# Kernel tuning notes

Measured on AMD Instinct MI355X. Metric: run time of the kernel, lower is better.

## Reference

```python
import jax, jax.numpy as jnp
from jax import lax
import numpy as np

H = 8          # n_heads
K = 4          # n_points == KNN k (hardcoded k=4 in original)
NN = 4         # neighbors per sampling point
D_MODEL = 256


def setup_inputs() -> dict:
    key = jax.random.key(0)
    ks = jax.random.split(key, 16)
    b, n_q, n_kv, d = 2, 1024, 2048, D_MODEL
    query = jax.random.normal(ks[0], (b, n_q, d), dtype=jnp.float32)
    query_pos = jax.random.uniform(ks[1], (b, n_q, 2), dtype=jnp.float32)
    key_value = jax.random.normal(ks[2], (b, n_kv, d), dtype=jnp.float32)
    kv_pos = jax.random.uniform(ks[3], (b, n_kv, 2), dtype=jnp.float32)
    # sampling_offsets linear: small weights + rotated-grid bias (as in _reset_parameters, scaled
    # so sampling locations stay near the unit square of kv positions)
    W_off = 0.001 * jax.random.normal(ks[4], (d, H * K * 2), dtype=jnp.float32)
    thetas = np.arange(H, dtype=np.float32) * (2.0 * np.pi / H)
    grid = np.stack([np.cos(thetas), np.sin(thetas)], -1)          # [H,2]
    grid = grid / np.abs(grid).max(-1, keepdims=True)
    grid = np.repeat(grid[:, None, :], K, axis=1)                  # [H,K,2]
    grid = grid * (np.arange(1, K + 1, dtype=np.float32)[None, :, None])
    b_off = jnp.asarray(0.05 * grid.reshape(-1), dtype=jnp.float32)
    W_attn = 0.02 * jax.random.normal(ks[5], (d, H * K), dtype=jnp.float32)
    b_attn = jnp.zeros((H * K,), dtype=jnp.float32)
    xav = (6.0 / (d + d)) ** 0.5
    W_v = jax.random.uniform(ks[6], (d, d), minval=-xav, maxval=xav, dtype=jnp.float32)
    b_v = jnp.zeros((d,), dtype=jnp.float32)
    W_out = jax.random.uniform(ks[7], (d, d), minval=-xav, maxval=xav, dtype=jnp.float32)
    b_out = jnp.zeros((d,), dtype=jnp.float32)
    shepard_power = jnp.asarray(1.0, dtype=jnp.float32)
    return {"query": query, "query_pos": query_pos, "key_value": key_value, "kv_pos": kv_pos,
            "W_off": W_off, "b_off": b_off, "W_attn": W_attn, "b_attn": b_attn,
            "W_v": W_v, "b_v": b_v, "W_out": W_out, "b_out": b_out,
            "shepard_power": shepard_power}


def _deform_attn(query, query_pos, key_value, kv_pos,
                 W_off, b_off, W_attn, b_attn, W_v, b_v, W_out, b_out, shepard_power):
    b, n_q, c = query.shape
    n_kv = key_value.shape[1]
    c_ = c // H
    # projections
    off = (query @ W_off + b_off).reshape(b, n_q, H, K, 2)
    attn = jax.nn.softmax((query @ W_attn + b_attn).reshape(b, n_q, H, K), axis=-1)
    values = (key_value @ W_v + b_v).reshape(b, n_kv, H, c_)
    values = values.transpose(0, 2, 1, 3).reshape(b * H, n_kv, c_)
    # sampling locations [b*H, n_q*K, 2]
    loc = (query_pos[:, :, None, None, :] + off).transpose(0, 2, 1, 3, 4)
    loc = loc.reshape(b * H, n_q * K, 2)
    kvp = jnp.broadcast_to(kv_pos[:, None], (b, H, n_kv, 2)).reshape(b * H, n_kv, 2)
    # brute-force KNN (k=4) on squared distances via GEMM expansion
    d2 = ((loc * loc).sum(-1)[:, :, None] + (kvp * kvp).sum(-1)[:, None, :]
          - 2.0 * jnp.einsum('bqd,bkd->bqk', loc, kvp))           # [bH, nqK, n_kv]
    _, nb_idx = lax.top_k(-d2, NN)                                 # [bH, nqK, 4]
    bidx = jnp.arange(b * H)[:, None, None]
    nb_pos = kvp[bidx, nb_idx]                                     # [bH, nqK, 4, 2]
    dist = jnp.linalg.norm(nb_pos - loc[:, :, None, :], axis=-1) + 1e-6
    power = jax.nn.relu(shepard_power) + 1e-6
    nn_w = jax.nn.softmax(-power * dist, axis=-1)                  # Shepard weights over 4 nbrs
    nn_w = nn_w.reshape(b * H, n_q, K, NN)
    idx = nb_idx.reshape(b * H, n_q, K, NN)
    attn_r = attn.transpose(0, 2, 1, 3).reshape(b * H, n_q, K)
    vg = values[jnp.arange(b * H)[:, None, None, None], idx]       # [bH, n_q, K, 4, c_]
    out = jnp.einsum('bqp,bqpn,bqpnc->bqc', attn_r, nn_w, vg)      # [bH, n_q, c_]
    out = out.reshape(b, H, n_q, c_).transpose(0, 2, 1, 3).reshape(b, n_q, c)
    return out @ W_out + b_out


def reference(query, query_pos, key_value, kv_pos,
              W_off, b_off, W_attn, b_attn, W_v, b_v, W_out, b_out, shepard_power):
    return _deform_attn(query, query_pos, key_value, kv_pos,
                        W_off, b_off, W_attn, b_attn, W_v, b_v, W_out, b_out, shepard_power)
```

## Files before the change

kernel.cpp:

```cpp
#include <hip/hip_runtime.h>
#include <math.h>

#define H 8
#define K 4
#define NN 4
#define D 256
#define NQ 1024
#define NKV 2048
#define BATCH 2
#define CH 32
#define GC 16
#define CELLH 0.0625f

#define OFF_LOC   0u
#define OFF_ATTN  524288u
#define OFF_VWS   786432u
#define OFF_HEAD  4980736u
#define OFF_PTS   7077888u
#define OFF_CST   7143424u
#define WS_NEED   7147520u

__global__ void k_offattn(const float* __restrict__ q, const float* __restrict__ qpos,
                          const float* __restrict__ Woff, const float* __restrict__ boff,
                          const float* __restrict__ Wattn, const float* __restrict__ battn,
                          float* __restrict__ loc, float* __restrict__ attnw) {
    int row = blockIdx.x;
    int b = row >> 10, qi = row & (NQ - 1);
    __shared__ float qs[D];
    for (int d = threadIdx.x; d < D; d += blockDim.x) qs[d] = q[(size_t)row * D + d];
    __syncthreads();
    int j = threadIdx.x;
    if (j < 64) {
        float acc = 0.0f;
        for (int d = 0; d < D; ++d) acc = fmaf(qs[d], Woff[d * 64 + j], acc);
        float off = acc + boff[j];
        int xy = j & 1;
        int hk = j >> 1;
        int h = hk >> 2, k = hk & 3;
        float L = qpos[(size_t)row * 2 + xy] + off;
        int g = ((b * H + h) * NQ + qi) * K + k;
        loc[(size_t)g * 2 + xy] = L;
    } else if (j < 96) {
        int j2 = j - 64;
        float acc = 0.0f;
        for (int d = 0; d < D; ++d) acc = fmaf(qs[d], Wattn[d * 32 + j2], acc);
        acc += battn[j2];
        float m = acc;
        m = fmaxf(m, __shfl_xor(m, 1));
        m = fmaxf(m, __shfl_xor(m, 2));
        float e = expf(acc - m);
        float s = e;
        s += __shfl_xor(s, 1);
        s += __shfl_xor(s, 2);
        float w = e / s;
        int h = j2 >> 2, k = j2 & 3;
        attnw[((b * H + h) * NQ + qi) * K + k] = w;
    }
}

__global__ void k_values(const float* __restrict__ kv, const float* __restrict__ Wv,
                         const float* __restrict__ bv, float* __restrict__ vws) {
    int r0 = blockIdx.x * 4;
    __shared__ float ks[4][D];
    for (int t = threadIdx.x; t < 4 * D; t += 256) ks[t >> 8][t & 255] = kv[(size_t)r0 * D + t];
    __syncthreads();
    int c = threadIdx.x;
    float a0 = 0.f, a1 = 0.f, a2 = 0.f, a3 = 0.f;
    for (int d = 0; d < D; ++d) {
        float w = Wv[d * D + c];
        a0 = fmaf(ks[0][d], w, a0); a1 = fmaf(ks[1][d], w, a1);
        a2 = fmaf(ks[2][d], w, a2); a3 = fmaf(ks[3][d], w, a3);
    }
    float bias = bv[c];
    a0 += bias; a1 += bias; a2 += bias; a3 += bias;
    int h = c >> 5, cc = c & 31;
    float va[4] = {a0, a1, a2, a3};
    for (int r = 0; r < 4; ++r) {
        int row = r0 + r;
        int b = row >> 11, n = row & (NKV - 1);
        vws[(((size_t)(b * H + h) * NKV) + n) * CH + cc] = va[r];
    }
}

__global__ void k_bin(const float* __restrict__ kvpos, float4* __restrict__ pts4,
                      int* __restrict__ cellStart) {
    #pragma clang fp contract(off)
    int b = blockIdx.x;
    int tid = threadIdx.x;
    __shared__ int cnt[GC * GC];
    __shared__ int ofs[GC * GC + 1];
    __shared__ int cur[GC * GC];
    if (tid < GC * GC) cnt[tid] = 0;
    __syncthreads();
    for (int n = tid; n < NKV; n += 256) {
        float x = kvpos[(size_t)(b * NKV + n) * 2 + 0];
        float y = kvpos[(size_t)(b * NKV + n) * 2 + 1];
        int ix = min(GC - 1, max(0, (int)floorf(x * (float)GC)));
        int iy = min(GC - 1, max(0, (int)floorf(y * (float)GC)));
        atomicAdd(&cnt[iy * GC + ix], 1);
    }
    __syncthreads();
    if (tid == 0) {
        int s = 0;
        for (int c = 0; c < GC * GC; ++c) { ofs[c] = s; s += cnt[c]; }
        ofs[GC * GC] = s;
    }
    __syncthreads();
    for (int t = tid; t < GC * GC + 1; t += 256) cellStart[b * 257 + t] = ofs[t];
    if (tid < GC * GC) cur[tid] = ofs[tid];
    __syncthreads();
    for (int n = tid; n < NKV; n += 256) {
        float x = kvpos[(size_t)(b * NKV + n) * 2 + 0];
        float y = kvpos[(size_t)(b * NKV + n) * 2 + 1];
        int ix = min(GC - 1, max(0, (int)floorf(x * (float)GC)));
        int iy = min(GC - 1, max(0, (int)floorf(y * (float)GC)));
        int pos = atomicAdd(&cur[iy * GC + ix], 1);
        pts4[(size_t)b * NKV + pos] = make_float4(-2.0f * x, -2.0f * y, x * x + y * y, (float)n);
    }
}

__device__ __forceinline__ void lexins(float t, int n,
                                       float& d0, float& d1, float& d2, float& d3,
                                       int& i0, int& i1, int& i2, int& i3) {
    bool c0 = (t < d0) || (t == d0 && n < i0);
    bool c1 = (t < d1) || (t == d1 && n < i1);
    bool c2 = (t < d2) || (t == d2 && n < i2);
    bool c3 = (t < d3) || (t == d3 && n < i3);
    d3 = c3 ? (c2 ? d2 : t) : d3;   i3 = c3 ? (c2 ? i2 : n) : i3;
    d2 = c2 ? (c1 ? d1 : t) : d2;   i2 = c2 ? (c1 ? i1 : n) : i2;
    d1 = c1 ? (c0 ? d0 : t) : d1;   i1 = c1 ? (c0 ? i0 : n) : i1;
    d0 = c0 ? t : d0;               i0 = c0 ? n : i0;
}

__device__ __forceinline__ void lexins_d(float t, int n,
                                         float& d0, float& d1, float& d2, float& d3,
                                         int& i0, int& i1, int& i2, int& i3) {
    bool nd = !((n == i0) | (n == i1) | (n == i2) | (n == i3));
    bool c0 = nd && ((t < d0) || (t == d0 && n < i0));
    bool c1 = nd && ((t < d1) || (t == d1 && n < i1));
    bool c2 = nd && ((t < d2) || (t == d2 && n < i2));
    bool c3 = nd && ((t < d3) || (t == d3 && n < i3));
    d3 = c3 ? (c2 ? d2 : t) : d3;   i3 = c3 ? (c2 ? i2 : n) : i3;
    d2 = c2 ? (c1 ? d1 : t) : d2;   i2 = c2 ? (c1 ? i1 : n) : i2;
    d1 = c1 ? (c0 ? d0 : t) : d1;   i1 = c1 ? (c0 ? i0 : n) : i1;
    d0 = c0 ? t : d0;               i0 = c0 ? n : i0;
}

__device__ __forceinline__ void bins4(float t, int n,
                                      float& d0, float& d1, float& d2, float& d3,
                                      int& i0, int& i1, int& i2, int& i3) {
    bool c0 = t < d0, c1 = t < d1, c2 = t < d2, c3 = t < d3;
    d3 = c3 ? (c2 ? d2 : t) : d3;   i3 = c3 ? (c2 ? i2 : n) : i3;
    d2 = c2 ? (c1 ? d1 : t) : d2;   i2 = c2 ? (c1 ? i1 : n) : i2;
    d1 = c1 ? (c0 ? d0 : t) : d1;   i1 = c1 ? (c0 ? i0 : n) : i1;
    d0 = c0 ? t : d0;               i0 = c0 ? n : i0;
}

__device__ __forceinline__ void knn_tail(int g, float lx, float ly,
                                         int i0, int i1, int i2, int i3,
                                         const float* __restrict__ kvpos,
                                         const float* __restrict__ attnw,
                                         const float* __restrict__ vws,
                                         float power, float* __restrict__ head) {
    #pragma clang fp contract(off)
    int bh = g >> 12;
    int b = bh >> 3, h = bh & 7;
    int qi = (g >> 2) & (NQ - 1);
    int k = g & 3;
    int idx[4] = {i0, i1, i2, i3};
    float z[4];
    #pragma unroll
    for (int u = 0; u < 4; ++u) {
        float kx = kvpos[(size_t)(b * NKV + idx[u]) * 2 + 0];
        float ky = kvpos[(size_t)(b * NKV + idx[u]) * 2 + 1];
        float dx = kx - lx;
        float dy = ky - ly;
        float dist = sqrtf(dx * dx + dy * dy) + 1e-6f;
        z[u] = -power * dist;
    }
    float m = fmaxf(fmaxf(z[0], z[1]), fmaxf(z[2], z[3]));
    float e0 = expf(z[0] - m), e1 = expf(z[1] - m), e2 = expf(z[2] - m), e3 = expf(z[3] - m);
    float esum = e0 + e1 + e2 + e3;
    float w0 = e0 / esum, w1 = e1 / esum, w2 = e2 / esum, w3 = e3 / esum;

    const float4* vp0 = (const float4*)(vws + ((size_t)bh * NKV + i0) * CH);
    const float4* vp1 = (const float4*)(vws + ((size_t)bh * NKV + i1) * CH);
    const float4* vp2 = (const float4*)(vws + ((size_t)bh * NKV + i2) * CH);
    const float4* vp3 = (const float4*)(vws + ((size_t)bh * NKV + i3) * CH);
    float a = attnw[g];
    float4 acc[8];
    #pragma unroll
    for (int t = 0; t < 8; ++t) {
        float4 x0 = vp0[t], x1 = vp1[t], x2 = vp2[t], x3 = vp3[t];
        float4 r;
        r.x = a * (w0 * x0.x + w1 * x1.x + w2 * x2.x + w3 * x3.x);
        r.y = a * (w0 * x0.y + w1 * x1.y + w2 * x2.y + w3 * x3.y);
        r.z = a * (w0 * x0.z + w1 * x1.z + w2 * x2.z + w3 * x3.z);
        r.w = a * (w0 * x0.w + w1 * x1.w + w2 * x2.w + w3 * x3.w);
        r.x += __shfl_xor(r.x, 1); r.x += __shfl_xor(r.x, 2);
        r.y += __shfl_xor(r.y, 1); r.y += __shfl_xor(r.y, 2);
        r.z += __shfl_xor(r.z, 1); r.z += __shfl_xor(r.z, 2);
        r.w += __shfl_xor(r.w, 1); r.w += __shfl_xor(r.w, 2);
        acc[t] = r;
    }
    float4* hp = (float4*)(head + ((size_t)(b * NQ + qi)) * D + h * CH);
    hp[k * 2]     = acc[k * 2];
    hp[k * 2 + 1] = acc[k * 2 + 1];
}

__global__ void k_knn_grid2(const float* __restrict__ kvpos, const float* __restrict__ loc,
                            const float* __restrict__ attnw, const float* __restrict__ vws,
                            const float* __restrict__ sp,
                            const float4* __restrict__ pts4, const int* __restrict__ cellStart,
                            float* __restrict__ head) {
    #pragma clang fp contract(off)
    int lane = threadIdx.x;
    int s = lane & 7;
    int g = blockIdx.x * 32 + (lane >> 3);
    int b = g >> 15;
    int bh = g >> 12;

    __shared__ int cst[GC * GC + 1];
    for (int i = threadIdx.x; i < GC * GC + 1; i += 256) cst[i] = cellStart[b * 257 + i];
    __syncthreads();

    const float4* gp = pts4 + (size_t)b * NKV;

    const float2* lp = (const float2*)loc;
    float2 L = lp[g];
    float lx = L.x, ly = L.y;
    float sl = lx * lx + ly * ly;

    int ix = min(GC - 1, max(0, (int)floorf(lx * (float)GC)));
    int iy = min(GC - 1, max(0, (int)floorf(ly * (float)GC)));

    float d0 = 1e30f, d1 = 1e30f, d2 = 1e30f, d3 = 1e30f;
    int i0 = 0x7FFFFFFF, i1 = 0x7FFFFFFF, i2 = 0x7FFFFFFF, i3 = 0x7FFFFFFF;

#define INS1(P) { float tt = (sl + (P).z) + fmaf(ly, (P).y, lx * (P).x);      \
                  lexins(tt, (int)(P).w, d0, d1, d2, d3, i0, i1, i2, i3); }

    {
        int bx0 = max(ix - 1, 0), bx1 = min(ix + 1, GC - 1);
        int by0 = max(iy - 1, 0), by1 = min(iy + 1, GC - 1);
        int a0 = cst[by0 * GC + bx0];
        int l0 = cst[by0 * GC + bx1 + 1] - a0;
        int a1 = 0, l1 = 0, a2 = 0, l2 = 0;
        if (by0 + 1 <= by1) { a1 = cst[(by0 + 1) * GC + bx0]; l1 = cst[(by0 + 1) * GC + bx1 + 1] - a1; }
        if (by0 + 2 <= by1) { a2 = cst[(by0 + 2) * GC + bx0]; l2 = cst[(by0 + 2) * GC + bx1 + 1] - a2; }
        int l01 = l0 + l1;
        int m = l01 + l2;
        int f = s;
        for (; f + 24 < m; f += 32) {
            int f0 = f, f1 = f + 8, f2 = f + 16, f3 = f + 24;
            int j0 = f0 < l0 ? a0 + f0 : (f0 < l01 ? a1 + (f0 - l0) : a2 + (f0 - l01));
            int j1 = f1 < l0 ? a0 + f1 : (f1 < l01 ? a1 + (f1 - l0) : a2 + (f1 - l01));
            int j2 = f2 < l0 ? a0 + f2 : (f2 < l01 ? a1 + (f2 - l0) : a2 + (f2 - l01));
            int j3 = f3 < l0 ? a0 + f3 : (f3 < l01 ? a1 + (f3 - l0) : a2 + (f3 - l01));
            float4 p0 = gp[j0], p1 = gp[j1], p2 = gp[j2], p3 = gp[j3];
            INS1(p0); INS1(p1); INS1(p2); INS1(p3);
        }
        for (; f < m; f += 8) {
            int j = f < l0 ? a0 + f : (f < l01 ? a1 + (f - l0) : a2 + (f - l01));
            float4 p = gp[j];
            INS1(p);
        }
    }

#define MERGE_P(M) {                                                           \
        float e0 = __shfl_xor(d0, M), e1 = __shfl_xor(d1, M);                  \
        float e2 = __shfl_xor(d2, M), e3 = __shfl_xor(d3, M);                  \
        int j0 = __shfl_xor(i0, M), j1 = __shfl_xor(i1, M);                    \
        int j2 = __shfl_xor(i2, M), j3 = __shfl_xor(i3, M);                    \
        lexins(e0, j0, d0, d1, d2, d3, i0, i1, i2, i3);                        \
        lexins(e1, j1, d0, d1, d2, d3, i0, i1, i2, i3);                        \
        lexins(e2, j2, d0, d1, d2, d3, i0, i1, i2, i3);                        \
        lexins(e3, j3, d0, d1, d2, d3, i0, i1, i2, i3);                        \
    }
#define MERGE_D(M) {                                                           \
        float e0 = __shfl_xor(d0, M), e1 = __shfl_xor(d1, M);                  \
        float e2 = __shfl_xor(d2, M), e3 = __shfl_xor(d3, M);                  \
        int j0 = __shfl_xor(i0, M), j1 = __shfl_xor(i1, M);                    \
        int j2 = __shfl_xor(i2, M), j3 = __shfl_xor(i3, M);                    \
        lexins_d(e0, j0, d0, d1, d2, d3, i0, i1, i2, i3);                      \
        lexins_d(e1, j1, d0, d1, d2, d3, i0, i1, i2, i3);                      \
        lexins_d(e2, j2, d0, d1, d2, d3, i0, i1, i2, i3);                      \
        lexins_d(e3, j3, d0, d1, d2, d3, i0, i1, i2, i3);                      \
    }

    MERGE_P(1);
    MERGE_P(2);
    MERGE_P(4);

    auto done_at = [&](int r) -> bool {
        int bx0 = ix - r, bx1 = ix + r, by0 = iy - r, by1 = iy + r;
        float bound = 1e30f;
        if (bx0 > 0)      bound = fminf(bound, lx - (float)bx0 * CELLH);
        if (bx1 < GC - 1) bound = fminf(bound, (float)(bx1 + 1) * CELLH - lx);
        if (by0 > 0)      bound = fminf(bound, ly - (float)by0 * CELLH);
        if (by1 < GC - 1) bound = fminf(bound, (float)(by1 + 1) * CELLH - ly);
        bool covered = (bx0 <= 0 && bx1 >= GC - 1 && by0 <= 0 && by1 >= GC - 1);
        return covered || (d3 < bound * bound - 1e-5f);
    };

#define SCAN_RANGE_S(JLO, JHI)                                       \
    for (int j = (JLO) + s; j < (JHI); j += 8) {                     \
        float4 p = gp[j];                                            \
        INS1(p);                                                     \
    }

    int r = 1;
    bool need = !done_at(1);
    while (__any(need)) {
        ++r;
        if (need) {
            int ry0 = iy - r, ry1 = iy + r;
            int rx0 = ix - r, rx1 = ix + r;
            int ca = max(rx0, 0), cb = min(rx1, GC - 1);
            if (ry0 >= 0)      { int base = ry0 * GC; SCAN_RANGE_S(cst[base + ca], cst[base + cb + 1]); }
            if (ry1 <= GC - 1) { int base = ry1 * GC; SCAN_RANGE_S(cst[base + ca], cst[base + cb + 1]); }
            int ya = max(ry0 + 1, 0), yb = min(ry1 - 1, GC - 1);
            if (rx0 >= 0)      for (int cy = ya; cy <= yb; ++cy) { int c = cy * GC + rx0; SCAN_RANGE_S(cst[c], cst[c + 1]); }
            if (rx1 <= GC - 1) for (int cy = ya; cy <= yb; ++cy) { int c = cy * GC + rx1; SCAN_RANGE_S(cst[c], cst[c + 1]); }
            MERGE_D(1);
            MERGE_D(2);
            MERGE_D(4);
            need = !done_at(r);
        }
    }
#undef SCAN_RANGE_S
#undef MERGE_P
#undef MERGE_D
#undef INS1

    int bb = bh >> 3, h = bh & 7;
    int qi = (g >> 2) & (NQ - 1);
    float power = fmaxf(sp[0], 0.0f) + 1e-6f;
    int idx[4] = {i0, i1, i2, i3};
    float z[4];
    #pragma unroll
    for (int u = 0; u < 4; ++u) {
        float kx = kvpos[(size_t)(bb * NKV + idx[u]) * 2 + 0];
        float ky = kvpos[(size_t)(bb * NKV + idx[u]) * 2 + 1];
        float dx = kx - lx;
        float dy = ky - ly;
        float dist = sqrtf(dx * dx + dy * dy) + 1e-6f;
        z[u] = -power * dist;
    }
    float m = fmaxf(fmaxf(z[0], z[1]), fmaxf(z[2], z[3]));
    float e0 = expf(z[0] - m), e1 = expf(z[1] - m), e2 = expf(z[2] - m), e3 = expf(z[3] - m);
    float esum = e0 + e1 + e2 + e3;
    float w0 = e0 / esum, w1 = e1 / esum, w2 = e2 / esum, w3 = e3 / esum;

    const float4* vp0 = (const float4*)(vws + ((size_t)bh * NKV + i0) * CH);
    const float4* vp1 = (const float4*)(vws + ((size_t)bh * NKV + i1) * CH);
    const float4* vp2 = (const float4*)(vws + ((size_t)bh * NKV + i2) * CH);
    const float4* vp3 = (const float4*)(vws + ((size_t)bh * NKV + i3) * CH);
    float a = attnw[g];
    float4* hp = (float4*)(head + ((size_t)(bb * NQ + qi)) * D + h * CH);
    {
        float4 x0 = vp0[s], x1 = vp1[s], x2 = vp2[s], x3 = vp3[s];
        float4 rr;
        rr.x = a * (w0 * x0.x + w1 * x1.x + w2 * x2.x + w3 * x3.x);
        rr.y = a * (w0 * x0.y + w1 * x1.y + w2 * x2.y + w3 * x3.y);
        rr.z = a * (w0 * x0.z + w1 * x1.z + w2 * x2.z + w3 * x3.z);
        rr.w = a * (w0 * x0.w + w1 * x1.w + w2 * x2.w + w3 * x3.w);
        rr.x += __shfl_xor(rr.x, 8); rr.x += __shfl_xor(rr.x, 16);
        rr.y += __shfl_xor(rr.y, 8); rr.y += __shfl_xor(rr.y, 16);
        rr.z += __shfl_xor(rr.z, 8); rr.z += __shfl_xor(rr.z, 16);
        rr.w += __shfl_xor(rr.w, 8); rr.w += __shfl_xor(rr.w, 16);
        if (((lane >> 3) & 3) == 0) hp[s] = rr;
    }
}

__global__ void k_knn_fused(const float* __restrict__ kvpos, const float* __restrict__ loc,
                            const float* __restrict__ attnw, const float* __restrict__ vws,
                            const float* __restrict__ sp, float* __restrict__ head) {
    #pragma clang fp contract(off)
    int g = blockIdx.x * 256 + threadIdx.x;
    int bh = g >> 12;
    int b = bh >> 3;
    __shared__ float sx[NKV];
    __shared__ float sy[NKV];
    __shared__ float sz[NKV];
    for (int n = threadIdx.x; n < NKV; n += 256) {
        float x = kvpos[(size_t)(b * NKV + n) * 2 + 0];
        float y = kvpos[(size_t)(b * NKV + n) * 2 + 1];
        sx[n] = -2.0f * x;
        sy[n] = -2.0f * y;
        sz[n] = x * x + y * y;
    }
    __syncthreads();
    const float2* lp = (const float2*)loc;
    float2 L = lp[g];
    float lx = L.x, ly = L.y;
    float sl = lx * lx + ly * ly;
    const float4* x4 = (const float4*)sx;
    const float4* y4 = (const float4*)sy;
    const float4* z4 = (const float4*)sz;
    float d0 = 1e30f, d1 = 1e30f, d2 = 1e30f, d3 = 1e30f;
    int i0 = 0, i1 = 0, i2 = 0, i3 = 0;
    for (int n = 0; n < NKV; n += 4) {
        int v = n >> 2;
        float4 xA = x4[v], yA = y4[v], zA = z4[v];
        float t0 = (sl + zA.x) + fmaf(ly, yA.x, lx * xA.x);
        float t1 = (sl + zA.y) + fmaf(ly, yA.y, lx * xA.y);
        float t2 = (sl + zA.z) + fmaf(ly, yA.z, lx * xA.z);
        float t3 = (sl + zA.w) + fmaf(ly, yA.w, lx * xA.w);
        bins4(t0, n + 0, d0, d1, d2, d3, i0, i1, i2, i3);
        bins4(t1, n + 1, d0, d1, d2, d3, i0, i1, i2, i3);
        bins4(t2, n + 2, d0, d1, d2, d3, i0, i1, i2, i3);
        bins4(t3, n + 3, d0, d1, d2, d3, i0, i1, i2, i3);
    }
    float power = fmaxf(sp[0], 0.0f) + 1e-6f;
    knn_tail(g, lx, ly, i0, i1, i2, i3, kvpos, attnw, vws, power, head);
}

__global__ void k_out(const float* __restrict__ head, const float* __restrict__ Wout,
                      const float* __restrict__ bout, float* __restrict__ out) {
    int r0 = blockIdx.x * 4;
    __shared__ float hs[4][D];
    for (int t = threadIdx.x; t < 4 * D; t += 256) hs[t >> 8][t & 255] = head[(size_t)r0 * D + t];
    __syncthreads();
    int c = threadIdx.x;
    float a0 = 0.f, a1 = 0.f, a2 = 0.f, a3 = 0.f;
    for (int d = 0; d < D; ++d) {
        float w = Wout[d * D + c];
        a0 = fmaf(hs[0][d], w, a0); a1 = fmaf(hs[1][d], w, a1);
        a2 = fmaf(hs[2][d], w, a2); a3 = fmaf(hs[3][d], w, a3);
    }
    float bias = bout[c];
    out[(size_t)(r0 + 0) * D + c] = a0 + bias;
    out[(size_t)(r0 + 1) * D + c] = a1 + bias;
    out[(size_t)(r0 + 2) * D + c] = a2 + bias;
    out[(size_t)(r0 + 3) * D + c] = a3 + bias;
}

extern "C" void kernel_launch(void* const* d_in, const int* in_sizes, int n_in,
                              void* d_out, int out_size, void* d_ws, size_t ws_size,
                              hipStream_t stream) {
    (void)in_sizes; (void)n_in; (void)out_size;
    const float* q     = (const float*)d_in[0];
    const float* qpos  = (const float*)d_in[1];
    const float* kv    = (const float*)d_in[2];
    const float* kvp   = (const float*)d_in[3];
    const float* Woff  = (const float*)d_in[4];
    const float* boff  = (const float*)d_in[5];
    const float* Wattn = (const float*)d_in[6];
    const float* battn = (const float*)d_in[7];
    const float* Wv    = (const float*)d_in[8];
    const float* bv    = (const float*)d_in[9];
    const float* Wout  = (const float*)d_in[10];
    const float* bout  = (const float*)d_in[11];
    const float* sp    = (const float*)d_in[12];
    float* out = (float*)d_out;

    char* ws = (char*)d_ws;
    float* loc      = (float*)(ws + OFF_LOC);
    float* attnw    = (float*)(ws + OFF_ATTN);
    float* vws      = (float*)(ws + OFF_VWS);
    float* head     = (float*)(ws + OFF_HEAD);
    float4* pts4    = (float4*)(ws + OFF_PTS);
    int* cellStart  = (int*)(ws + OFF_CST);

    hipLaunchKernelGGL(k_offattn, dim3(BATCH * NQ), dim3(128), 0, stream,
                       q, qpos, Woff, boff, Wattn, battn, loc, attnw);
    hipLaunchKernelGGL(k_values, dim3(BATCH * NKV / 4), dim3(256), 0, stream,
                       kv, Wv, bv, vws);
    if (ws_size >= (size_t)WS_NEED) {
        hipLaunchKernelGGL(k_bin, dim3(BATCH), dim3(256), 0, stream,
                           kvp, pts4, cellStart);
        hipLaunchKernelGGL(k_knn_grid2, dim3(BATCH * H * NQ * K / 32), dim3(256), 0, stream,
                           kvp, loc, attnw, vws, sp, pts4, cellStart, head);
    } else {
        hipLaunchKernelGGL(k_knn_fused, dim3(BATCH * H * NQ * K / 256), dim3(256), 0, stream,
                           kvp, loc, attnw, vws, sp, head);
    }
    hipLaunchKernelGGL(k_out, dim3(BATCH * NQ / 4), dim3(256), 0, stream,
                       head, Wout, bout, out);
}
```

Baseline: 119.5 us.

## Fuse binning into offset/attention kernel and register-tile the projection GEMMs

Merges the kv-position binning into the offset/attention projection kernel as extra blocks, which removes one launch. It also processes 8 query rows per block so each weight load is reused across rows. The value and output projection kernels now compute 16 rows per block, with each thread accumulating a 4x4 register tile from float4 weight loads, which cuts repeated weight traffic. The visible diff deletes k_knn_fused but the fallback launch still references it; it is likely moved within the elided region, though it might not be.

```diff
diff --git a/kernel.cpp b/kernel.cpp
--- a/kernel.cpp
+++ b/kernel.cpp
@@ -19,105 +19,6 @@
 #define OFF_PTS   7077888u
 #define OFF_CST   7143424u
 #define WS_NEED   7147520u
-
-__global__ void k_offattn(const float* __restrict__ q, const float* __restrict__ qpos,
-                          const float* __restrict__ Woff, const float* __restrict__ boff,
-                          const float* __restrict__ Wattn, const float* __restrict__ battn,
-                          float* __restrict__ loc, float* __restrict__ attnw) {
-    int row = blockIdx.x;
-    int b = row >> 10, qi = row & (NQ - 1);
-    __shared__ float qs[D];
-    for (int d = threadIdx.x; d < D; d += blockDim.x) qs[d] = q[(size_t)row * D + d];
-    __syncthreads();
-    int j = threadIdx.x;
-    if (j < 64) {
-        float acc = 0.0f;
-        for (int d = 0; d < D; ++d) acc = fmaf(qs[d], Woff[d * 64 + j], acc);
-        float off = acc + boff[j];
-        int xy = j & 1;
-        int hk = j >> 1;
-        int h = hk >> 2, k = hk & 3;
-        float L = qpos[(size_t)row * 2 + xy] + off;
-        int g = ((b * H + h) * NQ + qi) * K + k;
-        loc[(size_t)g * 2 + xy] = L;
-    } else if (j < 96) {
-        int j2 = j - 64;
-        float acc = 0.0f;
-        for (int d = 0; d < D; ++d) acc = fmaf(qs[d], Wattn[d * 32 + j2], acc);
-        acc += battn[j2];
-        float m = acc;
-        m = fmaxf(m, __shfl_xor(m, 1));
-        m = fmaxf(m, __shfl_xor(m, 2));
-        float e = expf(acc - m);
-        float s = e;
-        s += __shfl_xor(s, 1);
-        s += __shfl_xor(s, 2);
-        float w = e / s;
-        int h = j2 >> 2, k = j2 & 3;
-        attnw[((b * H + h) * NQ + qi) * K + k] = w;
-    }
-}
-
-__global__ void k_values(const float* __restrict__ kv, const float* __restrict__ Wv,
-                         const float* __restrict__ bv, float* __restrict__ vws) {
-    int r0 = blockIdx.x * 4;
-    __shared__ float ks[4][D];
-    for (int t = threadIdx.x; t < 4 * D; t += 256) ks[t >> 8][t & 255] = kv[(size_t)r0 * D + t];
-    __syncthreads();
-    int c = threadIdx.x;
-    float a0 = 0.f, a1 = 0.f, a2 = 0.f, a3 = 0.f;
-    for (int d = 0; d < D; ++d) {
-        float w = Wv[d * D + c];
-        a0 = fmaf(ks[0][d], w, a0); a1 = fmaf(ks[1][d], w, a1);
-        a2 = fmaf(ks[2][d], w, a2); a3 = fmaf(ks[3][d], w, a3);
-    }
-    float bias = bv[c];
-    a0 += bias; a1 += bias; a2 += bias; a3 += bias;
-    int h = c >> 5, cc = c & 31;
-    float va[4] = {a0, a1, a2, a3};
-    for (int r = 0; r < 4; ++r) {
-        int row = r0 + r;
-        int b = row >> 11, n = row & (NKV - 1);
-        vws[(((size_t)(b * H + h) * NKV) + n) * CH + cc] = va[r];
-    }
-}
-
-__global__ void k_bin(const float* __restrict__ kvpos, float4* __restrict__ pts4,
-                      int* __restrict__ cellStart) {
-    #pragma clang fp contract(off)
-    int b = blockIdx.x;
-    int tid = threadIdx.x;
-    __shared__ int cnt[GC * GC];
-    __shared__ int ofs[GC * GC + 1];
-    __shared__ int cur[GC * GC];
-    if (tid < GC * GC) cnt[tid] = 0;
-    __syncthreads();
-    for (int n = tid; n < NKV; n += 256) {
-        float x = kvpos[(size_t)(b * NKV + n) * 2 + 0];
-        float y = kvpos[(size_t)(b * NKV + n) * 2 + 1];
-        int ix = min(GC - 1, max(0, (int)floorf(x * (float)GC)));
-        int iy = min(GC - 1, max(0, (int)floorf(y * (float)GC)));
-        atomicAdd(&cnt[iy * GC + ix], 1);
-    }
-    __syncthreads();
-    if (tid == 0) {
-        int s = 0;
-        for (int c = 0; c < GC * GC; ++c) { ofs[c] = s; s += cnt[c]; }
-        ofs[GC * GC] = s;
-    }
-    __syncthreads();
-    for (int t = tid; t < GC * GC + 1; t += 256) cellStart[b * 257 + t] = ofs[t];
-    if (tid < GC * GC) cur[tid] = ofs[tid];
-    __syncthreads();
-    for (int n = tid; n < NKV; n += 256) {
-        float x = kvpos[(size_t)(b * NKV + n) * 2 + 0];
-        float y = kvpos[(size_t)(b * NKV + n) * 2 + 1];
-        int ix = min(GC - 1, max(0, (int)floorf(x * (float)GC)));
-        int iy = min(GC - 1, max(0, (int)floorf(y * (float)GC)));
-        int pos = atomicAdd(&cur[iy * GC + ix], 1);
-        pts4[(size_t)b * NKV + pos] = make_float4(-2.0f * x, -2.0f * y, x * x + y * y, (float)n);
-    }
-}
 
 __device__ __forceinline__ void lexins(float t, int n,
                                        float& d0, float& d1, float& d2, float& d3,
@@ -156,15 +57,338 @@
     d0 = c0 ? t : d0;               i0 = c0 ? n : i0;
 }
 
-__device__ __forceinline__ void knn_tail(int g, float lx, float ly,
-                                         int i0, int i1, int i2, int i3,
-                                         const float* __restrict__ kvpos,
-                                         const float* __restrict__ attnw,
-                                         const float* __restrict__ vws,
-                                         float power, float* __restrict__ head) {
+__global__ void k_offattn_bin(const float* __restrict__ q, const float* __restrict__ qpos,
+                              const float* __restrict__ Woff, const float* __restrict__ boff,
+                              const float* __restrict__ Wattn, const float* __restrict__ battn,
+                              const float* __restrict__ kvpos,
+                              float* __restrict__ loc, float* __restrict__ attnw,
+                              float4* __restrict__ pts4, int* __restrict__ cellStart) {
     #pragma clang fp contract(off)
+    if (blockIdx.x >= (BATCH * NQ) / 8) {
+        int b = blockIdx.x - (BATCH * NQ) / 8;
+        int tid = threadIdx.x;
+        __shared__ int cnt[GC * GC];
+        __shared__ int ofs[GC * GC + 1];
+        __shared__ int cur[GC * GC];
+        for (int c = tid; c < GC * GC; c += 128) cnt[c] = 0;
+        __syncthreads();
+        for (int n = tid; n < NKV; n += 128) {
+            float x = kvpos[(size_t)(b * NKV + n) * 2 + 0];
+            float y = kvpos[(size_t)(b * NKV + n) * 2 + 1];
+            int cix = min(GC - 1, max(0, (int)floorf(x * (float)GC)));
+            int ciy = min(GC - 1, max(0, (int)floorf(y * (float)GC)));
+            atomicAdd(&cnt[ciy * GC + cix], 1);
+        }
+        __syncthreads();
+        if (tid == 0) {
+            int s = 0;
+            for (int c = 0; c < GC * GC; ++c) { ofs[c] = s; s += cnt[c]; }
+            ofs[GC * GC] = s;
+        }
+        __syncthreads();
+        for (int t = tid; t < GC * GC + 1; t += 128) cellStart[b * 257 + t] = ofs[t];
+        for (int c = tid; c < GC * GC; c += 128) cur[c] = ofs[c];
+        __syncthreads();
+        for (int n = tid; n < NKV; n += 128) {
+            float x = kvpos[(size_t)(b * NKV + n) * 2 + 0];
+            float y = kvpos[(size_t)(b * NKV + n) * 2 + 1];
+            int cix = min(GC - 1, max(0, (int)floorf(x * (float)GC)));
+            int ciy = min(GC - 1, max(0, (int)floorf(y * (float)GC)));
+            int pos = atomicAdd(&cur[ciy * GC + cix], 1);
+            pts4[(size_t)b * NKV + pos] = make_float4(-2.0f * x, -2.0f * y, x * x + y * y, (float)n);
+        }
+        return;
+    }
+    int r0 = blockIdx.x * 8;
+    __shared__ float qs[8][D];
+    for (int t = threadIdx.x; t < 8 * D; t += 128) qs[t >> 8][t & 255] = q[(size_t)r0 * D + t];
+    __syncthreads();
+    int j = threadIdx.x;
+    if (j < 64) {
+        float acc[8];
+        #pragma unroll
+        for (int r = 0; r < 8; ++r) acc[r] = 0.0f;
+        for (int d = 0; d < D; ++d) {
+            float w = Woff[d * 64 + j];
+            #pragma unroll
+            for (int r = 0; r < 8; ++r) acc[r] = fmaf(qs[r][d], w, acc[r]);
+        }
+        float bo = boff[j];
+        int xy = j & 1;
+        int hk = j >> 1;
+        int h = hk >> 2, k = hk & 3;
+        #pragma unroll
+        for (int r = 0; r < 8; ++r) {
+            int row = r0 + r;
+            int b = row >> 10, qi = row & (NQ - 1);
+            float L = qpos[(size_t)row * 2 + xy] + (acc[r] + bo);
+            int g = ((b * H + h) * NQ + qi) * K + k;
+            loc[(size_t)g * 2 + xy] = L;
+        }
+    } else if (j < 96) {
+        int j2 = j - 64;
+        float acc[8];
+        #pragma unroll
+        for (int r = 0; r < 8; ++r) acc[r] = 0.0f;
+        for (int d = 0; d < D; ++d) {
+            float w = Wattn[d * 32 + j2];
+            #pragma unroll
+            for (int r = 0; r < 8; ++r) acc[r] = fmaf(qs[r][d], w, acc[r]);
+        }
+        float ba = battn[j2];
+        int h = j2 >> 2, k = j2 & 3;
+        #pragma unroll
+        for (int r = 0; r < 8; ++r) {
+            int row = r0 + r;
+            int b = row >> 10, qi = row & (NQ - 1);
+            float a = acc[r] + ba;
+            float m = a;
+            m = fmaxf(m, __shfl_xor(m, 1));
+            m = fmaxf(m, __shfl_xor(m, 2));
+            float e = expf(a - m);
+            float s = e;
+            s += __shfl_xor(s, 1);
+            s += __shfl_xor(s, 2);
+            attnw[((b * H + h) * NQ + qi) * K + k] = e / s;
+        }
+    }
+}
+
+__global__ void k_values(const float* __restrict__ kv, const float* __restrict__ Wv,
+                         const float* __restrict__ bv, float* __restrict__ vws) {
+    int r0 = blockIdx.x * 16;
+    __shared__ float ks[16][D];
+    for (int t = threadIdx.x; t < 16 * D; t += 256) ks[t >> 8][t & 255] = kv[(size_t)r0 * D + t];
+    __syncthreads();
+    int cg = threadIdx.x & 63;
+    int rg = threadIdx.x >> 6;
+    float4 a0 = {0,0,0,0}, a1 = {0,0,0,0}, a2 = {0,0,0,0}, a3 = {0,0,0,0};
+    for (int d = 0; d < D; ++d) {
+        float4 w = *(const float4*)&Wv[d * D + cg * 4];
+        float k0 = ks[rg * 4 + 0][d], k1 = ks[rg * 4 + 1][d];
+        float k2 = ks[rg * 4 + 2][d], k3 = ks[rg * 4 + 3][d];
+        a0.x = fmaf(k0, w.x, a0.x); a0.y = fmaf(k0, w.y, a0.y); a0.z = fmaf(k0, w.z, a0.z); a0.w = fmaf(k0, w.w, a0.w);
+        a1.x = fmaf(k1, w.x, a1.x); a1.y = fmaf(k1, w.y, a1.y); a1.z = fmaf(k1, w.z, a1.z); a1.w = fmaf(k1, w.w, a1.w);
+        a2.x = fmaf(k2, w.x, a2.x); a2.y = fmaf(k2, w.y, a2.y); a2.z = fmaf(k2, w.z, a2.z); a2.w = fmaf(k2, w.w, a2.w);
+        a3.x = fmaf(k3, w.x, a3.x); a3.y = fmaf(k3, w.y, a3.y); a3.z = fmaf(k3, w.z, a3.z); a3.w = fmaf(k3, w.w, a3.w);
+    }
+    float4 bias = *(const float4*)&bv[cg * 4];
+    int c = cg * 4, h = c >> 5, cc = c & 31;
+    float4 va[4] = {a0, a1, a2, a3};
+    #pragma unroll
+    for (int rr = 0; rr < 4; ++rr) {
+        int row = r0 + rg * 4 + rr;
+        int b = row >> 11, n = row & (NKV - 1);
+        float4 v;
+        v.x = va[rr].x + bias.x; v.y = va[rr].y + bias.y;
+        v.z = va[rr].z + bias.z; v.w = va[rr].w + bias.w;
+        *(float4*)&vws[(((size_t)(b * H + h) * NKV) + n) * CH + cc] = v;
+    }
+}
+
+__global__ void k_knn_grid2(const float* __restrict__ kvpos, const float* __restrict__ loc,
+                            const float* __restrict__ attnw, const float* __restrict__ vws,
+                            const float* __restrict__ sp,
+                            const float4* __restrict__ pts4, const int* __restrict__ cellStart,
+                            float* __restrict__ head) {
+    #pragma clang fp contract(off)
+    int lane = threadIdx.x;
+    int s = lane & 7;
+    int g = blockIdx.x * 32 + (lane >> 3);
+    int b = g >> 15;
     int bh = g >> 12;
-    int b = bh >> 3, h = bh & 7;
+
+    __shared__ int cst[GC * GC + 1];
+    for (int i = threadIdx.x; i < GC * GC + 1; i += 256) cst[i] = cellStart[b * 257 + i];
+    __syncthreads();
+
+    const float4* gp = pts4 + (size_t)b * NKV;
+    float2 L = ((const float2*)loc)[g];
+    float lx = L.x, ly = L.y;
+    float sl = lx * lx + ly * ly;
+
+    int ix = min(GC - 1, max(0, (int)floorf(lx * (float)GC)));
+    int iy = min(GC - 1, max(0, (int)floorf(ly * (float)GC)));
+
+    float d0 = 1e30f, d1 = 1e30f, d2 = 1e30f, d3 = 1e30f;
+    int i0 = 0x7FFFFFFF, i1 = 0x7FFFFFFF, i2 = 0x7FFFFFFF, i3 = 0x7FFFFFFF;
+
+#define INS1(P) { float tt = (sl + (P).z) + fmaf(ly, (P).y, lx * (P).x);      \
+                  lexins(tt, (int)(P).w, d0, d1, d2, d3, i0, i1, i2, i3); }
+
+    {
+        int bx0 = max(ix - 1, 0), bx1 = min(ix + 1, GC - 1);
+        int by0 = max(iy - 1, 0), by1 = min(iy + 1, GC - 1);
+        int a0 = cst[by0 * GC + bx0];
+        int l0 = cst[by0 * GC + bx1 + 1] - a0;
+        int a1 = 0, l1 = 0, a2 = 0, l2 = 0;
+        if (by0 + 1 <= by1) { a1 = cst[(by0 + 1) * GC + bx0]; l1 = cst[(by0 + 1) * GC + bx1 + 1] - a1; }
+        if (by0 + 2 <= by1) { a2 = cst[(by0 + 2) * GC + bx0]; l2 = cst[(by0 + 2) * GC + bx1 + 1] - a2; }
+        int l01 = l0 + l1;
+        int m = l01 + l2;
+        int f = s;
+        for (; f + 24 < m; f += 32) {
+            int f0 = f, f1 = f + 8, f2 = f + 16, f3 = f + 24;
+            int j0 = f0 < l0 ? a0 + f0 : (f0 < l01 ? a1 + (f0 - l0) : a2 + (f0 - l01));
+            int j1 = f1 < l0 ? a0 + f1 : (f1 < l01 ? a1 + (f1 - l0) : a2 + (f1 - l01));
+            int j2 = f2 < l0 ? a0 + f2 : (f2 < l01 ? a1 + (f2 - l0) : a2 + (f2 - l01));
+            int j3 = f3 < l0 ? a0 + f3 : (f3 < l01 ? a1 + (f3 - l0) : a2 + (f3 - l01));
+            float4 p0 = gp[j0], p1 = gp[j1], p2 = gp[j2], p3 = gp[j3];
+            INS1(p0); INS1(p1); INS1(p2); INS1(p3);
+        }
+        for (; f < m; f += 8) {
+            int j = f < l0 ? a0 + f : (f < l01 ? a1 + (f - l0) : a2 + (f - l01));
+            float4 p = gp[j];
+            INS1(p);
+        }
+    }
+
+#define MERGE_P(M) {                                                           \
+        float e0 = __shfl_xor(d0, M), e1 = __shfl_xor(d1, M);                  \
+        float e2 = __shfl_xor(d2, M), e3 = __shfl_xor(d3, M);                  \
+        int j0 = __shfl_xor(i0, M), j1 = __shfl_xor(i1, M);                    \
+        int j2 = __shfl_xor(i2, M), j3 = __shfl_xor(i3, M);                    \
+        lexins(e0, j0, d0, d1, d2, d3, i0, i1, i2, i3);                        \
+        lexins(e1, j1, d0, d1, d2, d3, i0, i1, i2, i3);                        \
+        lexins(e2, j2, d0, d1, d2, d3, i0, i1, i2, i3);                        \
+        lexins(e3, j3, d0, d1, d2, d3, i0, i1, i2, i3);                        \
+    }
+#define MERGE_D(M) {                                                           \
+        float e0 = __shfl_xor(d0, M), e1 = __shfl_xor(d1, M);                  \
+        float e2 = __shfl_xor(d2, M), e3 = __shfl_xor(d3, M);                  \
+        int j0 = __shfl_xor(i0, M), j1 = __shfl_xor(i1, M);                    \
+        int j2 = __shfl_xor(i2, M), j3 = __shfl_xor(i3, M);                    \
+        lexins_d(e0, j0, d0, d1, d2, d3, i0, i1, i2, i3);                      \
+        lexins_d(e1, j1, d0, d1, d2, d3, i0, i1, i2, i3);                      \
+        lexins_d(e2, j2, d0, d1, d2, d3, i0, i1, i2, i3);                      \
+        lexins_d(e3, j3, d0, d1, d2, d3, i0, i1, i2, i3);                      \
+    }
+
+    MERGE_P(1);
+    MERGE_P(2);
+    MERGE_P(4);
+
+    auto done_at = [&](int r) -> bool {
+        int bx0 = ix - r, bx1 = ix + r, by0 = iy - r, by1 = iy + r;
+        float bound = 1e30f;
+        if (bx0 > 0)      bound = fminf(bound, lx - (float)bx0 * CELLH);
+        if (bx1 < GC - 1) bound = fminf(bound, (float)(bx1 + 1) * CELLH - lx);
+        if (by0 > 0)      bound = fminf(bound, ly - (float)by0 * CELLH);
+        if (by1 < GC - 1) bound = fminf(bound, (float)(by1 + 1) * CELLH - ly);
+        bool covered = (bx0 <= 0 && bx1 >= GC - 1 && by0 <= 0 && by1 >= GC - 1);
+        return covered || (d3 < bound * bound - 1e-5f);
+    };
+
+#define SCAN_RANGE_S(JLO, JHI)                                       \
+    for (int j = (JLO) + s; j < (JHI); j += 8) {                     \
+        float4 p = gp[j];                                            \
+        INS1(p);                                                     \
+    }
+
+    int r = 1;
+    bool need = !done_at(1);
+    while (__any(need)) {
+        ++r;
+        if (need) {
+            int ry0 = iy - r, ry1 = iy + r;
+            int rx0 = ix - r, rx1 = ix + r;
+            int ca = max(rx0, 0), cb = min(rx1, GC - 1);
+            if (ry0 >= 0)      { int base = ry0 * GC; SCAN_RANGE_S(cst[base + ca], cst[base + cb + 1]); }
+            if (ry1 <= GC - 1) { int base = ry1 * GC; SCAN_RANGE_S(cst[base + ca], cst[base + cb + 1]); }
+            int ya = max(ry0 + 1, 0), yb = min(ry1 - 1, GC - 1);
+            if (rx0 >= 0)      for (int cy = ya; cy <= yb; ++cy) { int c = cy * GC + rx0; SCAN_RANGE_S(cst[c], cst[c + 1]); }
+            if (rx1 <= GC - 1) for (int cy = ya; cy <= yb; ++cy) { int c = cy * GC + rx1; SCAN_RANGE_S(cst[c], cst[c + 1]); }
+            MERGE_D(1);
+            MERGE_D(2);
+            MERGE_D(4);
+            need = !done_at(r);
+        }
+    }
+#undef SCAN_RANGE_S
+#undef MERGE_P
+#undef MERGE_D
+#undef INS1
+
+    int bb = bh >> 3, h = bh & 7;
+    int qi = (g >> 2) & (NQ - 1);
+    float power = fmaxf(sp[0], 0.0f) + 1e-6f;
+    int idx[4] = {i0, i1, i2, i3};
+    float z[4];
+    #pragma unroll
+    for (int u = 0; u < 4; ++u) {
+        float kx = kvpos[(size_t)(bb * NKV + idx[u]) * 2 + 0];
+        float ky = kvpos[(size_t)(bb * NKV + idx[u]) * 2 + 1];
+        float dx = kx - lx;
+        float dy = ky - ly;
+        float dist = sqrtf(dx * dx + dy * dy) + 1e-6f;
+        z[u] = -power * dist;
+    }
+    float m = fmaxf(fmaxf(z[0], z[1]), fmaxf(z[2], z[3]));
+    float e0 = expf(z[0] - m), e1 = expf(z[1] - m), e2 = expf(z[2] - m), e3 = expf(z[3] - m);
+    float esum = e0 + e1 + e2 + e3;
+    float w0 = e0 / esum, w1 = e1 / esum, w2 = e2 / esum, w3 = e3 / esum;
+
+    const float4* vp0 = (const float4*)(vws + ((size_t)bh * NKV + i0) * CH);
+    const float4* vp1 = (const float4*)(vws + ((size_t)bh * NKV + i1) * CH);
+    const float4* vp2 = (const float4*)(vws + ((size_t)bh * NKV + i2) * CH);
+    const float4* vp3 = (const float4*)(vws + ((size_t)bh * NKV + i3) * CH);
+    float a = attnw[g];
+    float4* hp = (float4*)(head + ((size_t)(bb * NQ + qi)) * D + h * CH);
+    {
+        float4 x0 = vp0[s], x1 = vp1[s], x2 = vp2[s], x3 = vp3[s];
+        float4 rr;
+        rr.x = a * (w0 * x0.x + w1 * x1.x + w2 * x2.x + w3 * x3.x);
+        rr.y = a * (w0 * x0.y + w1 * x1.y + w2 * x2.y + w3 * x3.y);
+        rr.z = a * (w0 * x0.z + w1 * x1.z + w2 * x2.z + w3 * x3.z);
+        rr.w = a * (w0 * x0.w + w1 * x1.w + w2 * x2.w + w3 * x3.w);
+        rr.x += __shfl_xor(rr.x, 8); rr.x += __shfl_xor(rr.x, 16);
+        rr.y += __shfl_xor(rr.y, 8); rr.y += __shfl_xor(rr.y, 16);
+        rr.z += __shfl_xor(rr.z, 8); rr.z += __shfl_xor(rr.z, 16);
+        rr.w += __shfl_xor(rr.w, 8); rr.w += __shfl_xor(rr.w, 16);
+        if (((lane >> 3) & 3) == 0) hp[s] = rr;
+    }
+}
+
+__global__ void k_knn_fused(const float* __restrict__ kvpos, const float* __restrict__ loc,
+                            const float* __restrict__ attnw, const float* __restrict__ vws,
+                            const float* __restrict__ sp, float* __restrict__ head) {
+    #pragma clang fp contract(off)
+    int g = blockIdx.x * 256 + threadIdx.x;
+    int bh = g >> 12;
+    int b = bh >> 3;
+    __shared__ float sx[NKV];
+    __shared__ float sy[NKV];
+    __shared__ float sz[NKV];
+    for (int n = threadIdx.x; n < NKV; n += 256) {
+        float x = kvpos[(size_t)(b * NKV + n) * 2 + 0];
+        float y = kvpos[(size_t)(b * NKV + n) * 2 + 1];
+        sx[n] = -2.0f * x;
+        sy[n] = -2.0f * y;
+        sz[n] = x * x + y * y;
+    }
+    __syncthreads();
+    float2 L = ((const float2*)loc)[g];
+    float lx = L.x, ly = L.y;
+    float sl = lx * lx + ly * ly;
+    const float4* x4 = (const float4*)sx;
+    const float4* y4 = (const float4*)sy;
+    const float4* z4 = (const float4*)sz;
+    float d0 = 1e30f, d1 = 1e30f, d2 = 1e30f, d3 = 1e30f;
+    int i0 = 0, i1 = 0, i2 = 0, i3 = 0;
+    for (int n = 0; n < NKV; n += 4) {
+        int v = n >> 2;
+        float4 xA = x4[v], yA = y4[v], zA = z4[v];
+        float t0 = (sl + zA.x) + fmaf(ly, yA.x, lx * xA.x);
+        float t1 = (sl + zA.y) + fmaf(ly, yA.y, lx * xA.y);
+        float t2 = (sl + zA.z) + fmaf(ly, yA.z, lx * xA.z);
+        float t3 = (sl + zA.w) + fmaf(ly, yA.w, lx * xA.w);
+        bins4(t0, n + 0, d0, d1, d2, d3, i0, i1, i2, i3);
+        bins4(t1, n + 1, d0, d1, d2, d3, i0, i1, i2, i3);
+        bins4(t2, n + 2, d0, d1, d2, d3, i0, i1, i2, i3);
+        bins4(t3, n + 3, d0, d1, d2, d3, i0, i1, i2, i3);
+    }
+    float power = fmaxf(sp[0], 0.0f) + 1e-6f;
+    int h = bh & 7;
     int qi = (g >> 2) & (NQ - 1);
     int k = g & 3;
     int idx[4] = {i0, i1, i2, i3};
@@ -182,7 +406,6 @@
     float e0 = expf(z[0] - m), e1 = expf(z[1] - m), e2 = expf(z[2] - m), e3 = expf(z[3] - m);
     float esum = e0 + e1 + e2 + e3;
     float w0 = e0 / esum, w1 = e1 / esum, w2 = e2 / esum, w3 = e3 / esum;
-
     const float4* vp0 = (const float4*)(vws + ((size_t)bh * NKV + i0) * CH);
     const float4* vp1 = (const float4*)(vws + ((size_t)bh * NKV + i1) * CH);
     const float4* vp2 = (const float4*)(vws + ((size_t)bh * NKV + i2) * CH);
@@ -208,232 +431,34 @@
     hp[k * 2 + 1] = acc[k * 2 + 1];
 }
 
-__global__ void k_knn_grid2(const float* __restrict__ kvpos, const float* __restrict__ loc,
-                            const float* __restrict__ attnw, const float* __restrict__ vws,
-                            const float* __restrict__ sp,
-                            const float4* __restrict__ pts4, const int* __restrict__ cellStart,
-                            float* __restrict__ head) {
-    #pragma clang fp contract(off)
-    int lane = threadIdx.x;
-    int s = lane & 7;
-    int g = blockIdx.x * 32 + (lane >> 3);
-    int b = g >> 15;
-    int bh = g >> 12;
-
-    __shared__ int cst[GC * GC + 1];
-    for (int i = threadIdx.x; i < GC * GC + 1; i += 256) cst[i] = cellStart[b * 257 + i];
-    __syncthreads();
-
-    const float4* gp = pts4 + (size_t)b * NKV;
-
-    const float2* lp = (const float2*)loc;
-    float2 L = lp[g];
-    float lx = L.x, ly = L.y;
-    float sl = lx * lx + ly * ly;
-
-    int ix = min(GC - 1, max(0, (int)floorf(lx * (float)GC)));
-    int iy = min(GC - 1, max(0, (int)floorf(ly * (float)GC)));
-
-    float d0 = 1e30f, d1 = 1e30f, d2 = 1e30f, d3 = 1e30f;
-    int i0 = 0x7FFFFFFF, i1 = 0x7FFFFFFF, i2 = 0x7FFFFFFF, i3 = 0x7FFFFFFF;
-
-#define INS1(P) { float tt = (sl + (P).z) + fmaf(ly, (P).y, lx * (P).x);      \
-                  lexins(tt, (int)(P).w, d0, d1, d2, d3, i0, i1, i2, i3); }
-
-    {
-        int bx0 = max(ix - 1, 0), bx1 = min(ix + 1, GC - 1);
-        int by0 = max(iy - 1, 0), by1 = min(iy + 1, GC - 1);
-        int a0 = cst[by0 * GC + bx0];
-        int l0 = cst[by0 * GC + bx1 + 1] - a0;
-        int a1 = 0, l1 = 0, a2 = 0, l2 = 0;
-        if (by0 + 1 <= by1) { a1 = cst[(by0 + 1) * GC + bx0]; l1 = cst[(by0 + 1) * GC + bx1 + 1] - a1; }
-        if (by0 + 2 <= by1) { a2 = cst[(by0 + 2) * GC + bx0]; l2 = cst[(by0 + 2) * GC + bx1 + 1] - a2; }
-        int l01 = l0 + l1;
-        int m = l01 + l2;
-        int f = s;
-        for (; f + 24 < m; f += 32) {
-            int f0 = f, f1 = f + 8, f2 = f + 16, f3 = f + 24;
-            int j0 = f0 < l0 ? a0 + f0 : (f0 < l01 ? a1 + (f0 - l0) : a2 + (f0 - l01));
-            int j1 = f1 < l0 ? a0 + f1 : (f1 < l01 ? a1 + (f1 - l0) : a2 + (f1 - l01));
-            int j2 = f2 < l0 ? a0 + f2 : (f2 < l01 ? a1 + (f2 - l0) : a2 + (f2 - l01));
-            int j3 = f3 < l0 ? a0 + f3 : (f3 < l01 ? a1 + (f3 - l0) : a2 + (f3 - l01));
-            float4 p0 = gp[j0], p1 = gp[j1], p2 = gp[j2], p3 = gp[j3];
-            INS1(p0); INS1(p1); INS1(p2); INS1(p3);
-        }
-        for (; f < m; f += 8) {
-            int j = f < l0 ? a0 + f : (f < l01 ? a1 + (f - l0) : a2 + (f - l01));
-            float4 p = gp[j];
-            INS1(p);
-        }
-    }
-
-#define MERGE_P(M) {                                                           \
-        float e0 = __shfl_xor(d0, M), e1 = __shfl_xor(d1, M);                  \
-        float e2 = __shfl_xor(d2, M), e3 = __shfl_xor(d3, M);                  \
-        int j0 = __shfl_xor(i0, M), j1 = __shfl_xor(i1, M);                    \
-        int j2 = __shfl_xor(i2, M), j3 = __shfl_xor(i3, M);                    \
-        lexins(e0, j0, d0, d1, d2, d3, i0, i1, i2, i3);                        \
-        lexins(e1, j1, d0, d1, d2, d3, i0, i1, i2, i3);                        \
-        lexins(e2, j2, d0, d1, d2, d3, i0, i1, i2, i3);                        \
-        lexins(e3, j3, d0, d1, d2, d3, i0, i1, i2, i3);                        \
-    }
-#define MERGE_D(M) {                                                           \
-        float e0 = __shfl_xor(d0, M), e1 = __shfl_xor(d1, M);                  \
-        float e2 = __shfl_xor(d2, M), e3 = __shfl_xor(d3, M);                  \
-        int j0 = __shfl_xor(i0, M), j1 = __shfl_xor(i1, M);                    \
-        int j2 = __shfl_xor(i2, M), j3 = __shfl_xor(i3, M);                    \
-        lexins_d(e0, j0, d0, d1, d2, d3, i0, i1, i2, i3);                      \
-        lexins_d(e1, j1, d0, d1, d2, d3, i0, i1, i2, i3);                      \
-        lexins_d(e2, j2, d0, d1, d2, d3, i0, i1, i2, i3);                      \
-        lexins_d(e3, j3, d0, d1, d2, d3, i0, i1, i2, i3);                      \
-    }
-
-    MERGE_P(1);
-    MERGE_P(2);
-    MERGE_P(4);
-
-    auto done_at = [&](int r) -> bool {
-        int bx0 = ix - r, bx1 = ix + r, by0 = iy - r, by1 = iy + r;
-        float bound = 1e30f;
-        if (bx0 > 0)      bound = fminf(bound, lx - (float)bx0 * CELLH);
-        if (bx1 < GC - 1) bound = fminf(bound, (float)(bx1 + 1) * CELLH - lx);
-        if (by0 > 0)      bound = fminf(bound, ly - (float)by0 * CELLH);
-        if (by1 < GC - 1) bound = fminf(bound, (float)(by1 + 1) * CELLH - ly);
-        bool covered = (bx0 <= 0 && bx1 >= GC - 1 && by0 <= 0 && by1 >= GC - 1);
-        return covered || (d3 < bound * bound - 1e-5f);
-    };
-
-#define SCAN_RANGE_S(JLO, JHI)                                       \
-    for (int j = (JLO) + s; j < (JHI); j += 8) {                     \
-        float4 p = gp[j];                                            \
-        INS1(p);                                                     \
-    }
-
-    int r = 1;
-    bool need = !done_at(1);
-    while (__any(need)) {
-        ++r;
-        if (need) {
-            int ry0 = iy - r, ry1 = iy + r;
-            int rx0 = ix - r, rx1 = ix + r;
-            int ca = max(rx0, 0), cb = min(rx1, GC - 1);
-            if (ry0 >= 0)      { int base = ry0 * GC; SCAN_RANGE_S(cst[base + ca], cst[base + cb + 1]); }
-            if (ry1 <= GC - 1) { int base = ry1 * GC; SCAN_RANGE_S(cst[base + ca], cst[base + cb + 1]); }
-            int ya = max(ry0 + 1, 0), yb = min(ry1 - 1, GC - 1);
-            if (rx0 >= 0)      for (int cy = ya; cy <= yb; ++cy) { int c = cy * GC + rx0; SCAN_RANGE_S(cst[c], cst[c + 1]); }
-            if (rx1 <= GC - 1) for (int cy = ya; cy <= yb; ++cy) { int c = cy * GC + rx1; SCAN_RANGE_S(cst[c], cst[c + 1]); }
-            MERGE_D(1);
-            MERGE_D(2);
-            MERGE_D(4);
-            need = !done_at(r);
-        }
-    }
-#undef SCAN_RANGE_S
-#undef MERGE_P
-#undef MERGE_D
-#undef INS1
-
-    int bb = bh >> 3, h = bh & 7;
-    int qi = (g >> 2) & (NQ - 1);
-    float power = fmaxf(sp[0], 0.0f) + 1e-6f;
-    int idx[4] = {i0, i1, i2, i3};
-    float z[4];
-    #pragma unroll
-    for (int u = 0; u < 4; ++u) {
-        float kx = kvpos[(size_t)(bb * NKV + idx[u]) * 2 + 0];
-        float ky = kvpos[(size_t)(bb * NKV + idx[u]) * 2 + 1];
-        float dx = kx - lx;
-        float dy = ky - ly;
-        float dist = sqrtf(dx * dx + dy * dy) + 1e-6f;
-        z[u] = -power * dist;
-    }
-    float m = fmaxf(fmaxf(z[0], z[1]), fmaxf(z[2], z[3]));
-    float e0 = expf(z[0] - m), e1 = expf(z[1] - m), e2 = expf(z[2] - m), e3 = expf(z[3] - m);
-    float esum = e0 + e1 + e2 + e3;
-    float w0 = e0 / esum, w1 = e1 / esum, w2 = e2 / esum, w3 = e3 / esum;
-
-    const float4* vp0 = (const float4*)(vws + ((size_t)bh * NKV + i0) * CH);
-    const float4* vp1 = (const float4*)(vws + ((size_t)bh * NKV + i1) * CH);
-    const float4* vp2 = (const float4*)(vws + ((size_t)bh * NKV + i2) * CH);
-    const float4* vp3 = (const float4*)(vws + ((size_t)bh * NKV + i3) * CH);
-    float a = attnw[g];
-    float4* hp = (float4*)(head + ((size_t)(bb * NQ + qi)) * D + h * CH);
-    {
-        float4 x0 = vp0[s], x1 = vp1[s], x2 = vp2[s], x3 = vp3[s];
-        float4 rr;
-        rr.x = a * (w0 * x0.x + w1 * x1.x + w2 * x2.x + w3 * x3.x);
-        rr.y = a * (w0 * x0.y + w1 * x1.y + w2 * x2.y + w3 * x3.y);
-        rr.z = a * (w0 * x0.z + w1 * x1.z + w2 * x2.z + w3 * x3.z);
-        rr.w = a * (w0 * x0.w + w1 * x1.w + w2 * x2.w + w3 * x3.w);
-        rr.x += __shfl_xor(rr.x, 8); rr.x += __shfl_xor(rr.x, 16);
-        rr.y += __shfl_xor(rr.y, 8); rr.y += __shfl_xor(rr.y, 16);
-        rr.z += __shfl_xor(rr.z, 8); rr.z += __shfl_xor(rr.z, 16);
-        rr.w += __shfl_xor(rr.w, 8); rr.w += __shfl_xor(rr.w, 16);
-        if (((lane >> 3) & 3) == 0) hp[s] = rr;
-    }
-}
-
-__global__ void k_knn_fused(const float* __restrict__ kvpos, const float* __restrict__ loc,
-                            const float* __restrict__ attnw, const float* __restrict__ vws,
-                            const float* __restrict__ sp, float* __restrict__ head) {
-    #pragma clang fp contract(off)
-    int g = blockIdx.x * 256 + threadIdx.x;
-    int bh = g >> 12;
-    int b = bh >> 3;
-    __shared__ float sx[NKV];
-    __shared__ float sy[NKV];
-    __shared__ float sz[NKV];
-    for (int n = threadIdx.x; n < NKV; n += 256) {
-        float x = kvpos[(size_t)(b * NKV + n) * 2 + 0];
-        float y = kvpos[(size_t)(b * NKV + n) * 2 + 1];
-        sx[n] = -2.0f * x;
-        sy[n] = -2.0f * y;
-        sz[n] = x * x + y * y;
-    }
-    __syncthreads();
-    const float2* lp = (const float2*)loc;
-    float2 L = lp[g];
-    float lx = L.x, ly = L.y;
-    float sl = lx * lx + ly * ly;
-    const float4* x4 = (const float4*)sx;
-    const float4* y4 = (const float4*)sy;
-    const float4* z4 = (const float4*)sz;
-    float d0 = 1e30f, d1 = 1e30f, d2 = 1e30f, d3 = 1e30f;
-    int i0 = 0, i1 = 0, i2 = 0, i3 = 0;
-    for (int n = 0; n < NKV; n += 4) {
-        int v = n >> 2;
-        float4 xA = x4[v], yA = y4[v], zA = z4[v];
-        float t0 = (sl + zA.x) + fmaf(ly, yA.x, lx * xA.x);
-        float t1 = (sl + zA.y) + fmaf(ly, yA.y, lx * xA.y);
-        float t2 = (sl + zA.z) + fmaf(ly, yA.z, lx * xA.z);
-        float t3 = (sl + zA.w) + fmaf(ly, yA.w, lx * xA.w);
-        bins4(t0, n + 0, d0, d1, d2, d3, i0, i1, i2, i3);
-        bins4(t1, n + 1, d0, d1, d2, d3, i0, i1, i2, i3);
-        bins4(t2, n + 2, d0, d1, d2, d3, i0, i1, i2, i3);
-        bins4(t3, n + 3, d0, d1, d2, d3, i0, i1, i2, i3);
-    }
-    float power = fmaxf(sp[0], 0.0f) + 1e-6f;
-    knn_tail(g, lx, ly, i0, i1, i2, i3, kvpos, attnw, vws, power, head);
-}
-
 __global__ void k_out(const float* __restrict__ head, const float* __restrict__ Wout,
                       const float* __restrict__ bout, float* __restrict__ out) {
-    int r0 = blockIdx.x * 4;
-    __shared__ float hs[4][D];
-    for (int t = threadIdx.x; t < 4 * D; t += 256) hs[t >> 8][t & 255] = head[(size_t)r0 * D + t];
+    int r0 = blockIdx.x * 16;
+    __shared__ float hs[16][D];
+    for (int t = threadIdx.x; t < 16 * D; t += 256) hs[t >> 8][t & 255] = head[(size_t)r0 * D + t];
     __syncthreads();
-    int c = threadIdx.x;
-    float a0 = 0.f, a1 = 0.f, a2 = 0.f, a3 = 0.f;
+    int cg = threadIdx.x & 63;
+    int rg = threadIdx.x >> 6;
+    float4 a0 = {0,0,0,0}, a1 = {0,0,0,0}, a2 = {0,0,0,0}, a3 = {0,0,0,0};
     for (int d = 0; d < D; ++d) {
-        float w = Wout[d * D + c];
-        a0 = fmaf(hs[0][d], w, a0); a1 = fmaf(hs[1][d], w, a1);
-        a2 = fmaf(hs[2][d], w, a2); a3 = fmaf(hs[3][d], w, a3);
-    }
-    float bias = bout[c];
-    out[(size_t)(r0 + 0) * D + c] = a0 + bias;
-    out[(size_t)(r0 + 1) * D + c] = a1 + bias;
-    out[(size_t)(r0 + 2) * D + c] = a2 + bias;
-    out[(size_t)(r0 + 3) * D + c] = a3 + bias;
+        float4 w = *(const float4*)&Wout[d * D + cg * 4];
+        float k0 = hs[rg * 4 + 0][d], k1 = hs[rg * 4 + 1][d];
+        float k2 = hs[rg * 4 + 2][d], k3 = hs[rg * 4 + 3][d];
+        a0.x = fmaf(k0, w.x, a0.x); a0.y = fmaf(k0, w.y, a0.y); a0.z = fmaf(k0, w.z, a0.z); a0.w = fmaf(k0, w.w, a0.w);
+        a1.x = fmaf(k1, w.x, a1.x); a1.y = fmaf(k1, w.y, a1.y); a1.z = fmaf(k1, w.z, a1.z); a1.w = fmaf(k1, w.w, a1.w);
+        a2.x = fmaf(k2, w.x, a2.x); a2.y = fmaf(k2, w.y, a2.y); a2.z = fmaf(k2, w.z, a2.z); a2.w = fmaf(k2, w.w, a2.w);
+        a3.x = fmaf(k3, w.x, a3.x); a3.y = fmaf(k3, w.y, a3.y); a3.z = fmaf(k3, w.z, a3.z); a3.w = fmaf(k3, w.w, a3.w);
+    }
+    float4 bias = *(const float4*)&bout[cg * 4];
+    float4 va[4] = {a0, a1, a2, a3};
+    #pragma unroll
+    for (int rr = 0; rr < 4; ++rr) {
+        int row = r0 + rg * 4 + rr;
+        float4 v;
+        v.x = va[rr].x + bias.x; v.y = va[rr].y + bias.y;
+        v.z = va[rr].z + bias.z; v.w = va[rr].w + bias.w;
+        *(float4*)&out[(size_t)row * D + cg * 4] = v;
+    }
 }
 
 extern "C" void kernel_launch(void* const* d_in, const int* in_sizes, int n_in,
@@ -463,19 +488,19 @@
     float4* pts4    = (float4*)(ws + OFF_PTS);
     int* cellStart  = (int*)(ws + OFF_CST);
 
-    hipLaunchKernelGGL(k_offattn, dim3(BATCH * NQ), dim3(128), 0, stream,
-                       q, qpos, Woff, boff, Wattn, battn, loc, attnw);
-    hipLaunchKernelGGL(k_values, dim3(BATCH * NKV / 4), dim3(256), 0, stream,
+    bool grid_ok = ws_size >= (size_t)WS_NEED;
+    int nblk = (BATCH * NQ) / 8 + (grid_ok ? BATCH : 0);
+    hipLaunchKernelGGL(k_offattn_bin, dim3(nblk), dim3(128), 0, stream,
+                       q, qpos, Woff, boff, Wattn, battn, kvp, loc, attnw, pts4, cellStart);
+    hipLaunchKernelGGL(k_values, dim3(BATCH * NKV / 16), dim3(256), 0, stream,
                        kv, Wv, bv, vws);
-    if (ws_size >= (size_t)WS_NEED) {
-        hipLaunchKernelGGL(k_bin, dim3(BATCH), dim3(256), 0, stream,
-                           kvp, pts4, cellStart);
+    if (grid_ok) {
         hipLaunchKernelGGL(k_knn_grid2, dim3(BATCH * H * NQ * K / 32), dim3(256), 0, stream,
                            kvp, loc, attnw, vws, sp, pts4, cellStart, head);
     } else {
         hipLaunchKernelGGL(k_knn_fused, dim3(BATCH * H * NQ * K / 256), dim3(256), 0, stream,
                            kvp, loc, attnw, vws, sp, head);
     }
-    hipLaunchKernelGGL(k_out, dim3(BATCH * NQ / 4), dim3(256), 0, stream,
+    hipLaunchKernelGGL(k_out, dim3(BATCH * NQ / 16), dim3(256), 0, stream,
                        head, Wout, bout, out);
 }
```

Measured after the change: 138.4 us. 15.8% more time.
